# Optimization experiments

Measured on AMD Instinct MI355X. Metric: run time of the kernel, lower is better.

Reference implementation:

```python
import jax, jax.numpy as jnp
import numpy as np

SCALE = 1.0 / np.sqrt(64.0).astype(np.float32)  # module hardcodes 64**0.5

def setup_inputs() -> dict:
    key = jax.random.key(0)
    kx, kw = jax.random.split(key)
    B, S, D, O = 8, 2048, 768, 768
    x = jax.random.normal(kx, (B, S, D), dtype=jnp.float32)
    # keras 'uniform' initializer: U(-0.05, 0.05)
    kernel = jax.random.uniform(kw, (3, D, O), dtype=jnp.float32, minval=-0.05, maxval=0.05)
    return {"x": x, "kernel": kernel}

def reference(x, kernel):
    # x: [B,S,D], kernel: [3,D,O]
    WQ = jnp.einsum('bsd,do->bso', x, kernel[0])
    WK = jnp.einsum('bsd,do->bso', x, kernel[1])
    WV = jnp.einsum('bsd,do->bso', x, kernel[2])
    QK = jnp.einsum('bso,bto->bst', WQ, WK) * SCALE  # [B,S,S]
    A = jax.nn.softmax(QK, axis=-1)
    return jnp.einsum('bst,bto->bso', A, WV)
```

## Files before the change

kernel.cpp:

```cpp
#include <hip/hip_runtime.h>


typedef _Float16 f16;
typedef _Float16 f16x8 __attribute__((ext_vector_type(8)));
typedef _Float16 f16x4 __attribute__((ext_vector_type(4)));
typedef float f32x4 __attribute__((ext_vector_type(4)));

__device__ __forceinline__ void gload16(const void* g, void* l) {
    __builtin_amdgcn_global_load_lds((__attribute__((address_space(1))) void*)g,
                                     (__attribute__((address_space(3))) void*)l,
                                     16, 0, 0);
}

template <int MODE, typename OutT>
__global__ __launch_bounds__(256, 2)
void gemm_bt(const f16* __restrict__ A, const f16* __restrict__ B,
             OutT* __restrict__ C, float* R, int K, int lda, int ldb, int ldc,
             long sA, long sB, long sC)
{
    __shared__ __align__(16) f16 lA[128 * 64];
    __shared__ __align__(16) f16 lB[128 * 64];

    const int tid  = threadIdx.x;
    const int wave = tid >> 6;
    const int lane = tid & 63;

    const unsigned gx = gridDim.x, gy = gridDim.y;
    const unsigned nb = gx * gy * gridDim.z;
    unsigned lin = blockIdx.x + gx * (blockIdx.y + gy * blockIdx.z);
    if ((nb & 7u) == 0u) lin = (lin & 7u) * (nb >> 3) + (lin >> 3);
    const unsigned bx = lin % gx;
    const unsigned rem = lin / gx;
    const unsigned by = rem % gy;
    const unsigned bz = rem / gy;

    A += (long)bz * sA;
    B += (long)bz * sB;
    C += (long)bz * sC;

    const long row0 = (long)by * 128;
    const long col0 = (long)bx * 128;

    const int r0 = tid >> 3;
    const int cs = (((tid & 7) ^ (r0 & 7)) * 8);
    const f16* ag0 = A + (row0 +      r0) * lda + cs;
    const f16* ag1 = A + (row0 + 32 + r0) * lda + cs;
    const f16* ag2 = A + (row0 + 64 + r0) * lda + cs;
    const f16* ag3 = A + (row0 + 96 + r0) * lda + cs;
    const f16* bg0 = B + (col0 +      r0) * ldb + cs;
    const f16* bg1 = B + (col0 + 32 + r0) * ldb + cs;
    const f16* bg2 = B + (col0 + 64 + r0) * ldb + cs;
    const f16* bg3 = B + (col0 + 96 + r0) * ldb + cs;
    f16* lA0 = lA +        wave * 512;
    f16* lA1 = lA + 2048 + wave * 512;
    f16* lA2 = lA + 4096 + wave * 512;
    f16* lA3 = lA + 6144 + wave * 512;
    f16* lB0 = lB +        wave * 512;
    f16* lB1 = lB + 2048 + wave * 512;
    f16* lB2 = lB + 4096 + wave * 512;
    f16* lB3 = lB + 6144 + wave * 512;

    const int wm = wave >> 1, wn = wave & 1;
    const int fl = lane & 15;
    const int q  = lane >> 4;
    const int co = ((q ^ (fl & 7)) * 8);
    const f16* paw = lA + (wm * 64 + fl) * 64;
    const f16* pbw = lB + (wn * 64 + fl) * 64;

    f32x4 acc[4][4] = {};

    for (int k0 = 0; k0 < K; k0 += 64) {
        __syncthreads();
        gload16(ag0, lA0); gload16(ag1, lA1);
        gload16(ag2, lA2); gload16(ag3, lA3);
        gload16(bg0, lB0); gload16(bg1, lB1);
        gload16(bg2, lB2); gload16(bg3, lB3);
        ag0 += 64; ag1 += 64; ag2 += 64; ag3 += 64;
        bg0 += 64; bg1 += 64; bg2 += 64; bg3 += 64;
        __syncthreads();

#pragma unroll
        for (int kk = 0; kk < 64; kk += 32) {
            const int o = co ^ (kk == 0 ? 0 : 32);
            f16x8 a[4], b[4];
#pragma unroll
            for (int i = 0; i < 4; ++i)
                a[i] = *(const f16x8*)(paw + i * 1024 + o);
#pragma unroll
            for (int j = 0; j < 4; ++j)
                b[j] = *(const f16x8*)(pbw + j * 1024 + o);
#pragma unroll
            for (int i = 0; i < 4; ++i)
#pragma unroll
                for (int j = 0; j < 4; ++j)
                    acc[i][j] = __builtin_amdgcn_mfma_f32_16x16x32_f16(
                        a[i], b[j], acc[i][j], 0, 0, 0);
        }
    }

    const int rq = (lane >> 4) * 4;
    if (MODE != 0) R += (long)bz * 2048;
#pragma unroll
    for (int i = 0; i < 4; ++i) {
#pragma unroll
        for (int r = 0; r < 4; ++r) {
            const long row = row0 + wm * 64 + i * 16 + rq + r;
            if (MODE == 0) {
#pragma unroll
                for (int j = 0; j < 4; ++j) {
                    const long col = col0 + wn * 64 + j * 16 + fl;
                    C[row * ldc + col] = (OutT)acc[i][j][r];
                }
            } else if (MODE == 1) {
                float s = 0.f;
#pragma unroll
                for (int j = 0; j < 4; ++j) {
                    const long col = col0 + wn * 64 + j * 16 + fl;
                    float e = __expf(acc[i][j][r] * 0.125f - 12.0f);
                    C[row * ldc + col] = (OutT)e;
                    s += e;
                }
                s += __shfl_xor(s, 1, 16);
                s += __shfl_xor(s, 2, 16);
                s += __shfl_xor(s, 4, 16);
                s += __shfl_xor(s, 8, 16);
                if (fl == 0) atomicAdd(&R[row], s);
            } else {
                const float inv = 1.0f / R[row];
#pragma unroll
                for (int j = 0; j < 4; ++j) {
                    const long col = col0 + wn * 64 + j * 16 + fl;
                    C[row * ldc + col] = (OutT)(acc[i][j][r] * inv);
                }
            }
        }
    }
}

__global__ void cvt_f32_f16(const float* __restrict__ in, f16* __restrict__ out,
                            int n4)
{
    int i = blockIdx.x * blockDim.x + threadIdx.x;
    int stride = gridDim.x * blockDim.x;
    for (; i < n4; i += stride) {
        float4 v = ((const float4*)in)[i];
        f16x4 h;
        h[0] = (f16)v.x; h[1] = (f16)v.y; h[2] = (f16)v.z; h[3] = (f16)v.w;
        ((f16x4*)out)[i] = h;
    }
}

__global__ void wtrans(const float* __restrict__ w, f16* __restrict__ wT)
{
    __shared__ float t[32][33];
    const int h  = blockIdx.z;
    const int o0 = blockIdx.x * 32, d0 = blockIdx.y * 32;
    const int tx = threadIdx.x & 31, ty = threadIdx.x >> 5;
    const float* src = w + ((size_t)h * 768 + d0) * 768 + o0;
#pragma unroll
    for (int r = 0; r < 32; r += 8)
        t[ty + r][tx] = src[(size_t)(ty + r) * 768 + tx];
    __syncthreads();
    f16* dst = wT + ((size_t)h * 768 + o0) * 768 + d0;
#pragma unroll
    for (int r = 0; r < 32; r += 8)
        dst[(size_t)(ty + r) * 768 + tx] = (f16)t[tx][ty + r];
}

extern "C" void kernel_launch(void* const* d_in, const int* in_sizes, int n_in,
                              void* d_out, int out_size, void* d_ws, size_t ws_size,
                              hipStream_t stream)
{
    (void)in_sizes; (void)n_in; (void)out_size; (void)ws_size;
    const float* x = (const float*)d_in[0];
    const float* w = (const float*)d_in[1];
    float* out = (float*)d_out;

    const long NX = 12582912;
    const long NW = 1769472;
    f16* xh  = (f16*)d_ws;
    f16* wT  = xh + NX;
    f16* QKh = wT + NW;
    f16* Vt  = QKh + 2 * NX;
    f16* Sc  = Vt + NX;
    float* R = (float*)xh;

    cvt_f32_f16<<<2048, 256, 0, stream>>>(x, xh, (int)(NX / 4));
    wtrans<<<dim3(24, 24, 3), 256, 0, stream>>>(w, wT);

    gemm_bt<0, f16><<<dim3(12, 128, 1), 256, 0, stream>>>(
        xh, wT, QKh, nullptr, 768, 768, 768, 1536, 0, 0, 0);
    gemm_bt<0, f16><<<dim3(16, 6, 8), 256, 0, stream>>>(
        wT + 1179648, xh, Vt, nullptr, 768, 768, 768, 2048, 0, 1572864, 1572864);
    hipMemsetAsync(R, 0, 8 * 2048 * sizeof(float), stream);
    gemm_bt<1, f16><<<dim3(16, 16, 8), 256, 0, stream>>>(
        QKh, QKh + 768, Sc, R, 768, 1536, 1536, 2048, 3145728, 3145728, 4194304);
    gemm_bt<2, float><<<dim3(6, 16, 8), 256, 0, stream>>>(
        Sc, Vt, out, R, 2048, 2048, 2048, 768, 4194304, 1572864, 1572864);
}
```

Measured before the change: 304.9 us.

## Double-buffer LDS tiles in the GEMM kernel to overlap loads with MFMA

Each GEMM block now has two shared-memory buffers for its A and B tiles. It prefetches the first K-slice before the main loop, and on every iteration issues the global-to-LDS loads for the next slice before computing on the current one. This drops one barrier per iteration and lets memory latency hide behind the MFMA work. In exchange, LDS use per block doubles to 64KB, which could limit occupancy if it no longer fits two blocks per CU.

```diff
diff --git a/kernel.cpp b/kernel.cpp
--- a/kernel.cpp
+++ b/kernel.cpp
@@ -18,8 +18,8 @@
              OutT* __restrict__ C, float* R, int K, int lda, int ldb, int ldc,
              long sA, long sB, long sC)
 {
-    __shared__ __align__(16) f16 lA[128 * 64];
-    __shared__ __align__(16) f16 lB[128 * 64];
+    __shared__ __align__(16) f16 lA[2][128 * 64];
+    __shared__ __align__(16) f16 lB[2][128 * 64];
 
     const int tid  = threadIdx.x;
     const int wave = tid >> 6;
@@ -51,34 +51,41 @@
     const f16* bg1 = B + (col0 + 32 + r0) * ldb + cs;
     const f16* bg2 = B + (col0 + 64 + r0) * ldb + cs;
     const f16* bg3 = B + (col0 + 96 + r0) * ldb + cs;
-    f16* lA0 = lA +        wave * 512;
-    f16* lA1 = lA + 2048 + wave * 512;
-    f16* lA2 = lA + 4096 + wave * 512;
-    f16* lA3 = lA + 6144 + wave * 512;
-    f16* lB0 = lB +        wave * 512;
-    f16* lB1 = lB + 2048 + wave * 512;
-    f16* lB2 = lB + 4096 + wave * 512;
-    f16* lB3 = lB + 6144 + wave * 512;
+    const int wofs = wave * 512;
 
     const int wm = wave >> 1, wn = wave & 1;
     const int fl = lane & 15;
     const int q  = lane >> 4;
     const int co = ((q ^ (fl & 7)) * 8);
-    const f16* paw = lA + (wm * 64 + fl) * 64;
-    const f16* pbw = lB + (wn * 64 + fl) * 64;
 
     f32x4 acc[4][4] = {};
 
-    for (int k0 = 0; k0 < K; k0 += 64) {
-        __syncthreads();
-        gload16(ag0, lA0); gload16(ag1, lA1);
-        gload16(ag2, lA2); gload16(ag3, lA3);
-        gload16(bg0, lB0); gload16(bg1, lB1);
-        gload16(bg2, lB2); gload16(bg3, lB3);
+    const int niter = K >> 6;
+    {
+        f16* a = lA[0] + wofs;
+        f16* b = lB[0] + wofs;
+        gload16(ag0, a);        gload16(ag1, a + 2048);
+        gload16(ag2, a + 4096); gload16(ag3, a + 6144);
+        gload16(bg0, b);        gload16(bg1, b + 2048);
+        gload16(bg2, b + 4096); gload16(bg3, b + 6144);
         ag0 += 64; ag1 += 64; ag2 += 64; ag3 += 64;
         bg0 += 64; bg1 += 64; bg2 += 64; bg3 += 64;
+    }
+
+    for (int it = 0; it < niter; ++it) {
         __syncthreads();
-
+        if (it + 1 < niter) {
+            f16* a = lA[(it + 1) & 1] + wofs;
+            f16* b = lB[(it + 1) & 1] + wofs;
+            gload16(ag0, a);        gload16(ag1, a + 2048);
+            gload16(ag2, a + 4096); gload16(ag3, a + 6144);
+            gload16(bg0, b);        gload16(bg1, b + 2048);
+            gload16(bg2, b + 4096); gload16(bg3, b + 6144);
+            ag0 += 64; ag1 += 64; ag2 += 64; ag3 += 64;
+            bg0 += 64; bg1 += 64; bg2 += 64; bg3 += 64;
+        }
+        const f16* paw = lA[it & 1] + (wm * 64 + fl) * 64;
+        const f16* pbw = lB[it & 1] + (wn * 64 + fl) * 64;
 #pragma unroll
         for (int kk = 0; kk < 64; kk += 32) {
             const int o = co ^ (kk == 0 ? 0 : 32);
```

Measured after the change: 340.1 us. 11.5% more time.
